# Kernel optimization log

Hardware: AMD Instinct MI355X
Metric: run time of the kernel (lower is better)

## Reference

```python
import jax, jax.numpy as jnp
import numpy as np

S = 1    # support_num
K = 20   # KNN neighbor count for conv layers
B, V = 4, 4096


def _normalize(x, axis):
    n = jnp.linalg.norm(x, axis=axis, keepdims=True)
    return x / jnp.maximum(n, 1e-12)


def _knn(v, k):
    # v: (b, n, 3) -> (b, n, k) indices of k nearest (excluding self)
    sq = jnp.sum(v * v, axis=-1)
    dist = sq[:, :, None] + sq[:, None, :] - 2.0 * jnp.einsum('bic,bjc->bij', v, v)
    return jax.lax.top_k(-dist, k + 1)[1][:, :, 1:]


def _gather(feat, idx):
    # feat (b,n,c), idx (b,n,k) -> (b,n,k,c)
    return feat[jnp.arange(feat.shape[0])[:, None, None], idx]


def _dir_norm(verts, idx):
    nb = _gather(verts, idx)                       # (b,v,k,3)
    return _normalize(nb - verts[:, :, None, :], -1)


def _conv_surface(idx, verts, directions, kernel_num):
    b, v, k = idx.shape
    nd = _dir_norm(verts, idx)
    sd = _normalize(directions, 0)                 # (3, S*kernel_num)
    theta = jax.nn.relu(jnp.einsum('bvkc,cm->bvkm', nd, sd))
    theta = theta.reshape(b, v, k, S, kernel_num)
    return jnp.sum(jnp.max(theta, axis=2), axis=2)  # (b,v,kernel_num)


def _conv_layer(idx, verts, fm, W, bias, directions, out_c):
    b, v, k = idx.shape
    nd = _dir_norm(verts, idx)
    sd = _normalize(directions, 0)                 # (3, S*out_c)
    theta = jax.nn.relu(jnp.einsum('bvkc,cm->bvkm', nd, sd))  # (b,v,k,S*out_c)
    fo = fm @ W + bias                             # (b,v,(S+1)*out_c)
    center = fo[:, :, :out_c]
    support = _gather(fo[:, :, out_c:], idx)       # (b,v,k,S*out_c)
    act = (theta * support).reshape(b, v, k, S, out_c)
    return center + jnp.sum(jnp.max(act, axis=2), axis=2)


def _pool(verts, fm, rate, nn, seed):
    b, v, _ = verts.shape
    idx = _knn(verts, nn)
    pooled = jnp.max(_gather(fm, idx), axis=2)
    sel = jax.random.permutation(jax.random.key(seed), v)[: v // rate]
    return verts[:, sel, :], pooled[:, sel, :]


def _ln(x, g, b):
    m = jnp.mean(x, -1, keepdims=True)
    var = jnp.mean(jnp.square(x - m), -1, keepdims=True)
    return (x - m) / jnp.sqrt(var + 1e-6) * g + b


def _mha(q, kv, Win, bin_, Wout, bout, h):
    E = q.shape[-1]
    hd = E // h
    wq, wk, wv = jnp.split(Win, 3, axis=0)
    bq, bk, bv = jnp.split(bin_, 3)

    def heads(x, w, bb_):
        y = x @ w.T + bb_
        return y.reshape(y.shape[0], y.shape[1], h, hd).transpose(0, 2, 1, 3)

    qh, kh, vh = heads(q, wq, bq), heads(kv, wk, bk), heads(kv, wv, bv)
    a = jax.nn.softmax(jnp.einsum('bhqd,bhkd->bhqk', qh, kh) / jnp.sqrt(jnp.float32(hd)), -1)
    o = jnp.einsum('bhqk,bhkd->bhqd', a, vh).transpose(0, 2, 1, 3).reshape(q.shape)
    return o @ Wout.T + bout


def _conv1x1(x, W, b):
    # x (B,C,N,1) -> (B,O,N,1)
    return jnp.einsum('bcnl,oc->bonl', x, W) + b[None, :, None, None]


def _bn_train(x, g, b):
    # BatchNorm2d in training mode (batch statistics), eps=1e-5
    m = jnp.mean(x, axis=(0, 2, 3), keepdims=True)
    v = jnp.var(x, axis=(0, 2, 3), keepdims=True)
    return (x - m) / jnp.sqrt(v + 1e-5) * g[None, :, None, None] + b[None, :, None, None]


def _forward(vertices, d0, g0, be0, w1, b1, dir1, g1, be1, w2, b2, dir2, g2, be2,
             w3, b3, dir3, g3, be3, token, a1_in_w, a1_in_b, a1_out_w, a1_out_b,
             ffn1_w, ffn1_b, bg, bb, ffn2_w, ffn2_b, a2_in_w, a2_in_b, a2_out_w,
             a2_out_b, w7, b7, dir7, g4, be4, c8_w, c8_b):
    b = vertices.shape[0]
    v0 = vertices[:, 0]                                 # (b, 4096, 3)
    idx0 = _knn(v0, K)
    fm0 = jax.nn.relu(_ln(_conv_surface(idx0, v0, d0, 32), g0, be0))
    fm1 = jax.nn.relu(_ln(_conv_layer(idx0, v0, fm0, w1, b1, dir1, 64), g1, be1))
    v1, fm1 = _pool(v0, fm1, 4, 4, 1)                   # (b,1024,3), (b,1024,64)
    idx1 = _knn(v1, K)
    fm_x = fm1
    fm2 = jax.nn.relu(_ln(_conv_layer(idx1, v1, fm1, w2, b2, dir2, 128), g2, be2))
    fm3 = jax.nn.relu(_ln(_conv_layer(idx1, v1, fm2, w3, b3, dir3, 256), g3, be3))
    _, fm3 = _pool(v1, fm3, 4, 4, 2)                    # (b,256,256)
    tok = jnp.tile(token, (b, 1, 1, 1))[:, :, :, 0].transpose(0, 2, 1)  # (b,1024,64)
    query = _mha(tok, fm_x, a1_in_w, a1_in_b, a1_out_w, a1_out_b, 4) + fm_x
    q2 = query.transpose(0, 2, 1)[:, :, :, None]        # (b,64,1024,1)
    q2 = _conv1x1(jax.nn.relu(_bn_train(_conv1x1(q2, ffn1_w, ffn1_b), bg, bb)), ffn2_w, ffn2_b)
    query = q2[:, :, :, 0].transpose(0, 2, 1)           # (b,1024,256)
    cross = _mha(query, fm3, a2_in_w, a2_in_b, a2_out_w, a2_out_b, 4) + query
    fmf = jax.nn.relu(_ln(_conv_layer(idx1, v1, cross, w7, b7, dir7, 1024), g4, be4))
    fmf = fmf.transpose(0, 2, 1)[:, :, :, None]         # (b,1024,1024,1)
    return _conv1x1(fmf, c8_w, c8_b)                    # (b,256,1024,1)


def setup_inputs():
    ks = iter(jax.random.split(jax.random.key(0), 64))

    def rn(shape, s=0.05):
        return jax.random.normal(next(ks), shape, dtype=jnp.float32) * s

    f32 = jnp.float32
    return dict(
        vertices=jax.random.normal(next(ks), (B, 1, V, 3), dtype=f32),
        d0=rn((3, S * 32)), g0=jnp.ones((32,), f32), be0=jnp.zeros((32,), f32),
        w1=rn((32, (S + 1) * 64)), b1=rn(((S + 1) * 64,)), dir1=rn((3, S * 64)),
        g1=jnp.ones((64,), f32), be1=jnp.zeros((64,), f32),
        w2=rn((64, (S + 1) * 128)), b2=rn(((S + 1) * 128,)), dir2=rn((3, S * 128)),
        g2=jnp.ones((128,), f32), be2=jnp.zeros((128,), f32),
        w3=rn((128, (S + 1) * 256)), b3=rn(((S + 1) * 256,)), dir3=rn((3, S * 256)),
        g3=jnp.ones((256,), f32), be3=jnp.zeros((256,), f32),
        token=rn((1, 64, 1024, 1), 1.0),
        a1_in_w=rn((192, 64)), a1_in_b=rn((192,)), a1_out_w=rn((64, 64)), a1_out_b=rn((64,)),
        ffn1_w=rn((256, 64)), ffn1_b=rn((256,)), bg=jnp.ones((256,), f32), bb=jnp.zeros((256,), f32),
        ffn2_w=rn((256, 256)), ffn2_b=rn((256,)),
        a2_in_w=rn((768, 256)), a2_in_b=rn((768,)), a2_out_w=rn((256, 256)), a2_out_b=rn((256,)),
        w7=rn((256, (S + 1) * 1024)), b7=rn(((S + 1) * 1024,)), dir7=rn((3, S * 1024)),
        g4=jnp.ones((1024,), f32), be4=jnp.zeros((1024,), f32),
        c8_w=rn((256, 1024)), c8_b=rn((256,)),
    )


def reference(vertices, d0, g0, be0, w1, b1, dir1, g1, be1, w2, b2, dir2, g2, be2,
              w3, b3, dir3, g3, be3, token, a1_in_w, a1_in_b, a1_out_w, a1_out_b,
              ffn1_w, ffn1_b, bg, bb, ffn2_w, ffn2_b, a2_in_w, a2_in_b, a2_out_w,
              a2_out_b, w7, b7, dir7, g4, be4, c8_w, c8_b):
    return _forward(vertices, d0, g0, be0, w1, b1, dir1, g1, be1, w2, b2, dir2, g2,
                    be2, w3, b3, dir3, g3, be3, token, a1_in_w, a1_in_b, a1_out_w,
                    a1_out_b, ffn1_w, ffn1_b, bg, bb, ffn2_w, ffn2_b, a2_in_w,
                    a2_in_b, a2_out_w, a2_out_b, w7, b7, dir7, g4, be4, c8_w, c8_b)
```

## Files before the change

kernel.cpp:

```cpp
#include <hip/hip_runtime.h>
#include <stdint.h>
#include <stddef.h>

#define FINF __builtin_inff()

__device__ inline void tf2x32(uint32_t k0, uint32_t k1, uint32_t x0, uint32_t x1,
                              uint32_t* o0, uint32_t* o1) {
  uint32_t ks2 = k0 ^ k1 ^ 0x1BD11BDAu;
  uint32_t v0 = x0 + k0, v1 = x1 + k1;
#define TFR(r) { v0 += v1; v1 = (v1 << (r)) | (v1 >> (32 - (r))); v1 ^= v0; }
  TFR(13) TFR(15) TFR(26) TFR(6)
  v0 += k1;  v1 += ks2 + 1u;
  TFR(17) TFR(29) TFR(16) TFR(24)
  v0 += ks2; v1 += k0 + 2u;
  TFR(13) TFR(15) TFR(26) TFR(6)
  v0 += k0;  v1 += k1 + 3u;
  TFR(17) TFR(29) TFR(16) TFR(24)
  v0 += k1;  v1 += ks2 + 4u;
  TFR(13) TFR(15) TFR(26) TFR(6)
  v0 += ks2; v1 += k0 + 5u;
#undef TFR
  *o0 = v0; *o1 = v1;
}

__device__ inline void perm_subkey(uint32_t seed, int round, uint32_t* s0, uint32_t* s1) {
  uint32_t k0 = 0u, k1 = seed;
  for (int r = 0; r < round; r++) {
    uint32_t a0, a1; tf2x32(k0, k1, 0u, 0u, &a0, &a1);
    k0 = a0; k1 = a1;
  }
  tf2x32(k0, k1, 0u, 1u, s0, s1);
}

__global__ __launch_bounds__(256) void perm_pass_kernel(uint32_t seed, int round, int n,
                                                        const int* __restrict__ vin,
                                                        int* __restrict__ vout, int m) {
  __shared__ unsigned long long lk[4096];
  __shared__ int part[256];
  uint32_t s0, s1; perm_subkey(seed, round, &s0, &s1);
  int t = threadIdx.x;
  for (int j = t; j < n; j += 256) {
    uint32_t y0, y1; tf2x32(s0, s1, 0u, (uint32_t)j, &y0, &y1);
    lk[j] = ((unsigned long long)(y0 ^ y1) << 32) | (unsigned)j;
  }
  __syncthreads();
  int r = blockIdx.x * 64 + (t & 63);
  int q = t >> 6;
  unsigned long long ki = lk[r];
  int cnt = 0;
  int j0 = q * (n >> 2), j1 = j0 + (n >> 2);
  for (int j = j0; j < j1; j++) cnt += (lk[j] < ki) ? 1 : 0;
  part[t] = cnt;
  __syncthreads();
  if (t < 64) {
    int rank = part[t] + part[t + 64] + part[t + 128] + part[t + 192];
    if (rank < m) vout[rank] = vin ? vin[r] : r;
  }
}

__global__ __launch_bounds__(256) void perm_passA_kernel(int* __restrict__ pt1,
                                                         int* __restrict__ sel2) {
  __shared__ unsigned long long lk[4096];
  __shared__ int part[256];
  bool big = (blockIdx.x < 64);
  uint32_t seed = big ? 1u : 2u;
  int n = big ? 4096 : 1024;
  int m = big ? 4096 : 256;
  int* vout = big ? pt1 : sel2;
  int blk = big ? blockIdx.x : (blockIdx.x - 64);
  uint32_t s0, s1; perm_subkey(seed, 0, &s0, &s1);
  int t = threadIdx.x;
  for (int j = t; j < n; j += 256) {
    uint32_t y0, y1; tf2x32(s0, s1, 0u, (uint32_t)j, &y0, &y1);
    lk[j] = ((unsigned long long)(y0 ^ y1) << 32) | (unsigned)j;
  }
  __syncthreads();
  int r = blk * 64 + (t & 63);
  int q = t >> 6;
  unsigned long long ki = lk[r];
  int cnt = 0;
  int j0 = q * (n >> 2), j1 = j0 + (n >> 2);
  for (int j = j0; j < j1; j++) cnt += (lk[j] < ki) ? 1 : 0;
  part[t] = cnt;
  __syncthreads();
  if (t < 64) {
    int rank = part[t] + part[t + 64] + part[t + 128] + part[t + 192];
    if (rank < m) vout[rank] = r;
  }
}

__device__ inline void wave_argmin2(float head_d, int head_i, float* Mo, int* wio) {
  float M = head_d;
#pragma unroll
  for (int off = 1; off < 64; off <<= 1) M = fminf(M, __shfl_xor(M, off));
  int cand = (head_d == M) ? head_i : 0x7fffffff;
#pragma unroll
  for (int off = 1; off < 64; off <<= 1) cand = min(cand, __shfl_xor(cand, off));
  *Mo = M; *wio = cand;
}

template <int CNT, int WAVES>
__global__ __launch_bounds__(64 * WAVES) void knn_lex_kernel(const float* __restrict__ verts,
                                                             int N,
                                                             int* __restrict__ idx20,
                                                             int* __restrict__ idx4) {
  constexpr int SH = (CNT - 1 < 21) ? (CNT - 1) : 21;
  int row = blockIdx.x; int b = row / N, i = row - b * N;
  int t = threadIdx.x; int w = t >> 6; int lane = t & 63;
  const float* vb = verts + (size_t)b * N * 3;
  float xi = vb[i * 3], yi = vb[i * 3 + 1], zi = vb[i * 3 + 2];
  float sqi = (xi * xi + yi * yi) + zi * zi;

  int base = w * (N / WAVES) + lane;
  float qd[CNT]; int qi[CNT];
#pragma unroll
  for (int m = 0; m < CNT; m++) {
    int j = base + m * 64;
    float xj = vb[j * 3], yj = vb[j * 3 + 1], zj = vb[j * 3 + 2];
    float sqj = (xj * xj + yj * yj) + zj * zj;
    float dot = (xi * xj + yi * yj) + zi * zj;
    qd[m] = sqi + sqj - 2.f * dot;
    qi[m] = j;
  }
#pragma unroll
  for (int k = 2; k <= CNT; k <<= 1)
#pragma unroll
    for (int j = k >> 1; j > 0; j >>= 1)
#pragma unroll
      for (int m = 0; m < CNT; m++) {
        int l = m ^ j;
        if (l > m) {
          bool up = ((m & k) == 0);
          bool sw = up ? (qd[m] > qd[l]) : (qd[m] < qd[l]);
          float td = sw ? qd[l] : qd[m]; qd[l] = sw ? qd[m] : qd[l]; qd[m] = td;
          int ti = sw ? qi[l] : qi[m]; qi[l] = sw ? qi[m] : qi[l]; qi[m] = ti;
        }
      }

  __shared__ float wd[WAVES][21];
  __shared__ int wi[WAVES][21];
  for (int r = 0; r < 21; r++) {
    float M; int widx;
    wave_argmin2(qd[0], qi[0], &M, &widx);
    if (lane == 0) { wd[w][r] = M; wi[w][r] = widx; }
    bool win = (qi[0] == widx);
#pragma unroll
    for (int m = 0; m < SH; m++) {
      qd[m] = win ? qd[m + 1] : qd[m];
      qi[m] = win ? qi[m + 1] : qi[m];
    }
    if (SH == CNT - 1) {
      if (win) { qd[CNT - 1] = FINF; qi[CNT - 1] = 0x7fffffff; }
    }
  }
  __syncthreads();
  if (lane < 21) {
    float d0 = wd[w][lane]; int i0 = wi[w][lane];
    int rank = lane;
#pragma unroll
    for (int w2 = 0; w2 < WAVES; w2++) {
      if (w2 == w) continue;
      for (int p = 0; p < 21; p++) {
        float ld = wd[w2][p]; int li = wi[w2][p];
        rank += (ld < d0 || (ld == d0 && li < i0)) ? 1 : 0;
      }
    }
    if (rank >= 1 && rank <= 20) idx20[(size_t)row * 20 + (rank - 1)] = i0;
    if (rank >= 1 && rank <= 4)  idx4[(size_t)row * 4 + (rank - 1)] = i0;
  }
}

__global__ __launch_bounds__(256) void knnv1_w2_kernel(const float* __restrict__ verts,
                                                       int* __restrict__ idx20,
                                                       int* __restrict__ idx4,
                                                       const float* __restrict__ x,
                                                       const float* __restrict__ W,
                                                       const float* __restrict__ bias,
                                                       float* __restrict__ y) {
  if (blockIdx.x < 1024) {
    constexpr int CNT = 16;
    const int N = 1024;
    int lane = threadIdx.x & 63;
    int row = blockIdx.x * 4 + (threadIdx.x >> 6);
    int b = row / N, i = row - b * N;
    const float* vb = verts + (size_t)b * N * 3;
    float xi = vb[i * 3], yi = vb[i * 3 + 1], zi = vb[i * 3 + 2];
    float sqi = (xi * xi + yi * yi) + zi * zi;
    float qd[CNT]; int qi[CNT];
#pragma unroll
    for (int m = 0; m < CNT; m++) {
      int j = lane + m * 64;
      float xj = vb[j * 3], yj = vb[j * 3 + 1], zj = vb[j * 3 + 2];
      float sqj = (xj * xj + yj * yj) + zj * zj;
      float dot = (xi * xj + yi * yj) + zi * zj;
      qd[m] = sqi + sqj - 2.f * dot;
      qi[m] = j;
    }
#pragma unroll
    for (int k = 2; k <= CNT; k <<= 1)
#pragma unroll
      for (int j = k >> 1; j > 0; j >>= 1)
#pragma unroll
        for (int m = 0; m < CNT; m++) {
          int l = m ^ j;
          if (l > m) {
            bool up = ((m & k) == 0);
            bool sw = up ? (qd[m] > qd[l]) : (qd[m] < qd[l]);
            float td = sw ? qd[l] : qd[m]; qd[l] = sw ? qd[m] : qd[l]; qd[m] = td;
            int ti = sw ? qi[l] : qi[m]; qi[l] = sw ? qi[m] : qi[l]; qi[m] = ti;
          }
        }
    for (int r = 0; r < 21; r++) {
      float M; int widx;
      wave_argmin2(qd[0], qi[0], &M, &widx);
      if (lane == 0 && r >= 1) {
        idx20[(size_t)row * 20 + (r - 1)] = widx;
        if (r <= 4) idx4[(size_t)row * 4 + (r - 1)] = widx;
      }
      bool win = (qi[0] == widx);
#pragma unroll
      for (int m = 0; m < CNT - 1; m++) {
        qd[m] = win ? qd[m + 1] : qd[m];
        qi[m] = win ? qi[m + 1] : qi[m];
      }
      if (win) { qd[CNT - 1] = FINF; qi[CNT - 1] = 0x7fffffff; }
    }
  } else {
    const int I = 64, O = 256;
    int rb = (blockIdx.x - 1024) * 8;
    int o = threadIdx.x;
    __shared__ float xs[64][8];
    for (int u = 0; u < 8; u++)
      for (int i2 = threadIdx.x; i2 < I; i2 += 256) xs[i2][u] = x[(size_t)(rb + u) * I + i2];
    __syncthreads();
    float a[8] = {0, 0, 0, 0, 0, 0, 0, 0};
    for (int k2 = 0; k2 < I; k2++) {
      float wv = W[(size_t)k2 * O + o];
      float4 xa = *(const float4*)&xs[k2][0];
      float4 xb = *(const float4*)&xs[k2][4];
      a[0] += xa.x * wv; a[1] += xa.y * wv; a[2] += xa.z * wv; a[3] += xa.w * wv;
      a[4] += xb.x * wv; a[5] += xb.y * wv; a[6] += xb.z * wv; a[7] += xb.w * wv;
    }
    float bv = bias[o];
#pragma unroll
    for (int u = 0; u < 8; u++) y[(size_t)(rb + u) * O + o] = a[u] + bv;
  }
}

__global__ __launch_bounds__(256) void conv_surface_kernel(const float* __restrict__ verts,
                                                           const int* __restrict__ idx20,
                                                           const float* __restrict__ d0,
                                                           const float* __restrict__ g,
                                                           const float* __restrict__ be,
                                                           float* __restrict__ out, int N) {
  int w = threadIdx.x >> 6; int t = threadIdx.x & 63;
  int row = blockIdx.x * 4 + w; int b = row / N, i = row - b * N;
  __shared__ float nd[4][20][3];
  const float* vb = verts + (size_t)b * N * 3;
  if (t < 20) {
    int j = idx20[(size_t)row * 20 + t];
    float dx = vb[j * 3] - vb[i * 3], dy = vb[j * 3 + 1] - vb[i * 3 + 1], dz = vb[j * 3 + 2] - vb[i * 3 + 2];
    float n2 = sqrtf(dx * dx + dy * dy + dz * dz); n2 = fmaxf(n2, 1e-12f);
    nd[w][t][0] = dx / n2; nd[w][t][1] = dy / n2; nd[w][t][2] = dz / n2;
  }
  float x = 0.f;
  if (t < 32) {
    float a = d0[t], bb2 = d0[32 + t], c = d0[64 + t];
    float nrm = fmaxf(sqrtf(a * a + bb2 * bb2 + c * c), 1e-12f);
    a /= nrm; bb2 /= nrm; c /= nrm;
    float mx = -FINF;
    for (int kk = 0; kk < 20; kk++) {
      float th = fmaxf(nd[w][kk][0] * a + nd[w][kk][1] * bb2 + nd[w][kk][2] * c, 0.f);
      mx = fmaxf(mx, th);
    }
    x = mx;
  }
  float s = x;
  for (int off = 32; off; off >>= 1) s += __shfl_xor(s, off);
  float mean = s / 32.f;
  float dev = (t < 32) ? x - mean : 0.f;
  float s2 = dev * dev;
  for (int off = 32; off; off >>= 1) s2 += __shfl_xor(s2, off);
  float var = s2 / 32.f;
  if (t < 32) {
    float y = (x - mean) / sqrtf(var + 1e-6f) * g[t] + be[t];
    out[(size_t)row * 32 + t] = fmaxf(y, 0.f);
  }
}

__global__ void gemm_io_kernel(const float* __restrict__ x, const float* __restrict__ W,
                               const float* __restrict__ bias, float* __restrict__ y,
                               int R, int I, int O) {
  int rb = blockIdx.x * 8;
  int o = blockIdx.y * blockDim.x + threadIdx.x;
  __shared__ float xs[256][8];
  for (int u = 0; u < 8; u++)
    for (int i2 = threadIdx.x; i2 < I; i2 += blockDim.x) xs[i2][u] = x[(size_t)(rb + u) * I + i2];
  __syncthreads();
  float a[8] = {0, 0, 0, 0, 0, 0, 0, 0};
  for (int k2 = 0; k2 < I; k2++) {
    float wv = W[(size_t)k2 * O + o];
    float4 xa = *(const float4*)&xs[k2][0];
    float4 xb = *(const float4*)&xs[k2][4];
    a[0] += xa.x * wv; a[1] += xa.y * wv; a[2] += xa.z * wv; a[3] += xa.w * wv;
    a[4] += xb.x * wv; a[5] += xb.y * wv; a[6] += xb.z * wv; a[7] += xb.w * wv;
  }
  float bv = bias[o];
#pragma unroll
  for (int u = 0; u < 8; u++) y[(size_t)(rb + u) * O + o] = a[u] + bv;
}

__global__ void gemm_io16_kernel(const float* __restrict__ x, const float* __restrict__ W,
                                 const float* __restrict__ bias, float* __restrict__ y,
                                 int R, int I, int O) {
  int rb = blockIdx.x * 16;
  int o = blockIdx.y * blockDim.x + threadIdx.x;
  __shared__ float xs[256][16];
  for (int u = 0; u < 16; u++)
    for (int i2 = threadIdx.x; i2 < I; i2 += blockDim.x) xs[i2][u] = x[(size_t)(rb + u) * I + i2];
  __syncthreads();
  float a[16];
#pragma unroll
  for (int u = 0; u < 16; u++) a[u] = 0.f;
  for (int k2 = 0; k2 < I; k2++) {
    float wv = W[(size_t)k2 * O + o];
    float4 x0 = *(const float4*)&xs[k2][0];
    float4 x1 = *(const float4*)&xs[k2][4];
    float4 x2 = *(const float4*)&xs[k2][8];
    float4 x3 = *(const float4*)&xs[k2][12];
    a[0] += x0.x * wv; a[1] += x0.y * wv; a[2] += x0.z * wv; a[3] += x0.w * wv;
    a[4] += x1.x * wv; a[5] += x1.y * wv; a[6] += x1.z * wv; a[7] += x1.w * wv;
    a[8] += x2.x * wv; a[9] += x2.y * wv; a[10] += x2.z * wv; a[11] += x2.w * wv;
    a[12] += x3.x * wv; a[13] += x3.y * wv; a[14] += x3.z * wv; a[15] += x3.w * wv;
  }
  float bv = bias[o];
#pragma unroll
  for (int u = 0; u < 16; u++) y[(size_t)(rb + u) * O + o] = a[u] + bv;
}

template <int CPT>
__global__ void combine_kernel(const float* __restrict__ verts, const int* __restrict__ idx20,
                               const float* __restrict__ fo, const float* __restrict__ dirs,
                               const float* __restrict__ g, const float* __restrict__ be,
                               float* __restrict__ out, int N, int C) {
  int row = blockIdx.x; int b = row / N, i = row - b * N;
  int t = threadIdx.x, bs = blockDim.x;
  __shared__ float nd[20][3];
  __shared__ int nidx[20];
  __shared__ float red[8];
  const float* vb = verts + (size_t)b * N * 3;
  if (t < 20) {
    int j = idx20[(size_t)row * 20 + t];
    nidx[t] = j;
    float dx = vb[j * 3] - vb[i * 3], dy = vb[j * 3 + 1] - vb[i * 3 + 1], dz = vb[j * 3 + 2] - vb[i * 3 + 2];
    float n2 = fmaxf(sqrtf(dx * dx + dy * dy + dz * dz), 1e-12f);
    nd[t][0] = dx / n2; nd[t][1] = dy / n2; nd[t][2] = dz / n2;
  }
  __syncthreads();
  const float* fob = fo + (size_t)b * N * 2 * C;
  const float* forow = fob + (size_t)i * 2 * C;
  float da[CPT], db[CPT], dc[CPT], mx[CPT];
#pragma unroll
  for (int u = 0; u < CPT; u++) {
    int c = t + u * bs;
    float a = dirs[c], bb = dirs[C + c], cc = dirs[2 * C + c];
    float nrm = fmaxf(sqrtf(a * a + bb * bb + cc * cc), 1e-12f);
    da[u] = a / nrm; db[u] = bb / nrm; dc[u] = cc / nrm;
    mx[u] = -FINF;
  }
  for (int kk = 0; kk < 20; kk++) {
    float n0 = nd[kk][0], n1 = nd[kk][1], n2v = nd[kk][2];
    const float* sup = fob + (size_t)nidx[kk] * 2 * C + C + t;
#pragma unroll
    for (int u = 0; u < CPT; u++) {
      float th = fmaxf(n0 * da[u] + n1 * db[u] + n2v * dc[u], 0.f);
      mx[u] = fmaxf(mx[u], th * sup[u * bs]);
    }
  }
  float xv[CPT];
  float ssum = 0.f;
#pragma unroll
  for (int u = 0; u < CPT; u++) {
    int c = t + u * bs;
    float val = forow[c] + mx[u];
    xv[u] = val; ssum += val;
  }
  int nw = bs >> 6;
  for (int off = 32; off; off >>= 1) ssum += __shfl_down(ssum, off);
  if ((t & 63) == 0) red[t >> 6] = ssum;
  __syncthreads();
  if (t == 0) { float s = red[0]; for (int w = 1; w < nw; w++) s += red[w]; red[0] = s; }
  __syncthreads();
  float mean = red[0] / (float)C;
  __syncthreads();
  float s2 = 0.f;
#pragma unroll
  for (int u = 0; u < CPT; u++) { float d2 = xv[u] - mean; s2 += d2 * d2; }
  for (int off = 32; off; off >>= 1) s2 += __shfl_down(s2, off);
  if ((t & 63) == 0) red[t >> 6] = s2;
  __syncthreads();
  if (t == 0) { float s = red[0]; for (int w = 1; w < nw; w++) s += red[w]; red[0] = s; }
  __syncthreads();
  float inv = 1.0f / sqrtf(red[0] / (float)C + 1e-6f);
#pragma unroll
  for (int u = 0; u < CPT; u++) {
    int c = t + u * bs;
    float yv = (xv[u] - mean) * inv * g[c] + be[c];
    out[(size_t)row * C + c] = fmaxf(yv, 0.f);
  }
}

__global__ void pool_select_kernel(const float* __restrict__ fm, const int* __restrict__ idx4,
                                   const int* __restrict__ sel, const float* __restrict__ vin,
                                   float* __restrict__ vout, float* __restrict__ out,
                                   int N, int M, int C) {
  int row = blockIdx.x; int b = row / M, r = row - b * M;
  int s = sel[r];
  const int* id = idx4 + ((size_t)b * N + s) * 4;
  int i0 = id[0], i1 = id[1], i2 = id[2], i3 = id[3];
  const float* fb = fm + (size_t)b * N * C;
  for (int c = threadIdx.x; c < C; c += blockDim.x) {
    float m = fmaxf(fmaxf(fb[(size_t)i0 * C + c], fb[(size_t)i1 * C + c]),
                    fmaxf(fb[(size_t)i2 * C + c], fb[(size_t)i3 * C + c]));
    out[((size_t)b * M + r) * C + c] = m;
  }
  if (vout != nullptr && threadIdx.x < 3)
    vout[((size_t)b * M + r) * 3 + threadIdx.x] = vin[((size_t)b * N + s) * 3 + threadIdx.x];
}

__global__ void linear_oi_kernel(const float* __restrict__ x, const float* __restrict__ W,
                                 const float* __restrict__ bias, const float* __restrict__ res,
                                 float* __restrict__ y, int R, int I, int O) {
  int rb = blockIdx.x * 8;
  int o = threadIdx.x;
  __shared__ float xs[8][256];
  for (int u = 0; u < 8; u++)
    for (int i2 = threadIdx.x; i2 < I; i2 += O) xs[u][i2] = x[(size_t)(rb + u) * I + i2];
  __syncthreads();
  float a[8] = {0, 0, 0, 0, 0, 0, 0, 0};
  const float* w = W + (size_t)o * I;
  for (int k2 = 0; k2 < I; k2++) {
    float wv = w[k2];
#pragma unroll
    for (int u = 0; u < 8; u++) a[u] += xs[u][k2] * wv;
  }
  float bv = bias[o];
#pragma unroll
  for (int u = 0; u < 8; u++) {
    float val = a[u] + bv;
    if (res) val += res[(size_t)(rb + u) * O + o];
    y[(size_t)(rb + u) * O + o] = val;
  }
}

__global__ void linear_bn_kernel(const float* __restrict__ x, const float* __restrict__ W,
                                 const float* __restrict__ bias,
                                 const float* __restrict__ stats,
                                 const float* __restrict__ g, const float* __restrict__ b2,
                                 float* __restrict__ y, int R, int I, int O) {
  int rb = blockIdx.x * 8;
  int o = threadIdx.x;
  __shared__ float xs[8][256];
  for (int u = 0; u < 8; u++)
    for (int i2 = threadIdx.x; i2 < I; i2 += O) {
      float xr = x[(size_t)(rb + u) * I + i2];
      float yv = (xr - stats[i2]) / sqrtf(stats[I + i2] + 1e-5f) * g[i2] + b2[i2];
      xs[u][i2] = fmaxf(yv, 0.f);
    }
  __syncthreads();
  float a[8] = {0, 0, 0, 0, 0, 0, 0, 0};
  const float* w = W + (size_t)o * I;
  for (int k2 = 0; k2 < I; k2++) {
    float wv = w[k2];
#pragma unroll
    for (int u = 0; u < 8; u++) a[u] += xs[u][k2] * wv;
  }
  float bv = bias[o];
#pragma unroll
  for (int u = 0; u < 8; u++) y[(size_t)(rb + u) * O + o] = a[u] + bv;
}

__global__ __launch_bounds__(64) void qkv1_kernel(const float* __restrict__ token,
                                                  const float* __restrict__ fm1p,
                                                  const float* __restrict__ Win,
                                                  const float* __restrict__ bin,
                                                  float* __restrict__ Q1,
                                                  float* __restrict__ K1,
                                                  float* __restrict__ V1) {
  int ybr = blockIdx.y;
  const float* W = Win + (size_t)ybr * 64 * 64;
  const float* bias = bin + ybr * 64;
  float* out = (ybr == 0) ? Q1 : (ybr == 1) ? K1 : V1;
  int rb = blockIdx.x * 8;
  int o = threadIdx.x;
  __shared__ float xs[8][64];
  if (ybr == 0) {
    for (int u = 0; u < 8; u++) {
      int n = (rb + u) & 1023;
      xs[u][o] = token[(size_t)o * 1024 + n];
    }
  } else {
    for (int u = 0; u < 8; u++) xs[u][o] = fm1p[(size_t)(rb + u) * 64 + o];
  }
  __syncthreads();
  float a[8] = {0, 0, 0, 0, 0, 0, 0, 0};
  const float* w = W + (size_t)o * 64;
  for (int k2 = 0; k2 < 64; k2++) {
    float wv = w[k2];
#pragma unroll
    for (int u = 0; u < 8; u++) a[u] += xs[u][k2] * wv;
  }
  float bv = bias[o];
#pragma unroll
  for (int u = 0; u < 8; u++) out[(size_t)(rb + u) * 64 + o] = a[u] + bv;
}

__global__ __launch_bounds__(256) void kv2_kernel(const float* __restrict__ fm3p,
                                                  const float* __restrict__ Win,
                                                  const float* __restrict__ bin,
                                                  float* __restrict__ K2,
                                                  float* __restrict__ V2) {
  int ybr = blockIdx.y;
  const float* W = Win + (size_t)(1 + ybr) * 256 * 256;
  const float* bias = bin + (1 + ybr) * 256;
  float* out = ybr ? V2 : K2;
  int rb = blockIdx.x * 8;
  int o = threadIdx.x;
  __shared__ float xs[8][256];
  for (int u = 0; u < 8; u++) xs[u][o] = fm3p[(size_t)(rb + u) * 256 + o];
  __syncthreads();
  float a[8] = {0, 0, 0, 0, 0, 0, 0, 0};
  const float* w = W + (size_t)o * 256;
  for (int k2 = 0; k2 < 256; k2++) {
    float wv = w[k2];
#pragma unroll
    for (int u = 0; u < 8; u++) a[u] += xs[u][k2] * wv;
  }
  float bv = bias[o];
#pragma unroll
  for (int u = 0; u < 8; u++) out[(size_t)(rb + u) * 256 + o] = a[u] + bv;
}

template <int HD, int QPT, int KS>
__global__ __launch_bounds__(256) void attn_tiled(
    const float* __restrict__ q, const float* __restrict__ kk,
    const float* __restrict__ vv, float* __restrict__ o,
    int Lq, int Lk, int H, float scale) {
  constexpr int TK = 64;
  constexpr int QG = 256 / (2 * KS);
  constexpr int QPB = QG * QPT;
  constexpr int V4 = HD / 4;
  constexpr int STR = V4 + 1;
  constexpr int HH = HD / 2;
  constexpr int V4H = HH / 4;

  __shared__ float4 Ks[TK * STR];
  __shared__ float4 Vs[TK * STR];

  int t = threadIdx.x;
  int dh = t & 1;
  int ki = (t >> 1) & (KS - 1);
  int qg = t / (2 * KS);
  int nqt = Lq / QPB;
  int qt = blockIdx.x % nqt, bh = blockIdx.x / nqt;
  int h = bh % H, b = bh / H;
  int E = H * HD;
  int q0 = qt * QPB + qg * QPT;

  const float* qbase = q + ((size_t)b * Lq + q0) * E + h * HD + dh * HH;
  const float* kbase = kk + (size_t)b * Lk * E + h * HD;
  const float* vbase = vv + (size_t)b * Lk * E + h * HD;

  float qr[QPT][HH], O[QPT][HH], m[QPT], l[QPT];
#pragma unroll
  for (int r = 0; r < QPT; r++) {
    m[r] = -FINF; l[r] = 0.f;
#pragma unroll
    for (int d = 0; d < HH; d++) { qr[r][d] = qbase[(size_t)r * E + d]; O[r][d] = 0.f; }
  }

  for (int k0 = 0; k0 < Lk; k0 += TK) {
    __syncthreads();
    for (int e = t; e < TK * V4; e += 256) {
      int rr = e / V4, cc = e - rr * V4;
      Ks[rr * STR + cc] = *(const float4*)(kbase + (size_t)(k0 + rr) * E + cc * 4);
      Vs[rr * STR + cc] = *(const float4*)(vbase + (size_t)(k0 + rr) * E + cc * 4);
    }
    __syncthreads();
#pragma unroll 1
    for (int g = 0; g < TK / KS; g += 4) {
      float sc[QPT][4];
#pragma unroll
      for (int jj = 0; jj < 4; jj++) {
        int kl = (g + jj) * KS + ki;
        float sh[QPT];
#pragma unroll
        for (int r = 0; r < QPT; r++) sh[r] = 0.f;
        const float4* kr = &Ks[kl * STR + dh * V4H];
#pragma unroll
        for (int c = 0; c < V4H; c++) {
          float4 kv = kr[c];
#pragma unroll
          for (int r = 0; r < QPT; r++)
            sh[r] += qr[r][4 * c] * kv.x + qr[r][4 * c + 1] * kv.y
                   + qr[r][4 * c + 2] * kv.z + qr[r][4 * c + 3] * kv.w;
        }
#pragma unroll
        for (int r = 0; r < QPT; r++)
          sc[r][jj] = (sh[r] + __shfl_xor(sh[r], 1)) * scale;
      }
#pragma unroll
      for (int r = 0; r < QPT; r++) {
        float tm = fmaxf(fmaxf(sc[r][0], sc[r][1]), fmaxf(sc[r][2], sc[r][3]));
        float nm = fmaxf(m[r], tm);
        float a = __expf(m[r] - nm);
        m[r] = nm;
        float ls = l[r] * a;
#pragma unroll
        for (int d = 0; d < HH; d++) O[r][d] *= a;
#pragma unroll
        for (int jj = 0; jj < 4; jj++) { sc[r][jj] = __expf(sc[r][jj] - nm); ls += sc[r][jj]; }
        l[r] = ls;
      }
#pragma unroll
      for (int jj = 0; jj < 4; jj++) {
        int kl = (g + jj) * KS + ki;
        const float4* vr = &Vs[kl * STR + dh * V4H];
#pragma unroll
        for (int c = 0; c < V4H; c++) {
          float4 v4 = vr[c];
#pragma unroll
          for (int r = 0; r < QPT; r++) {
            O[r][4 * c]     += sc[r][jj] * v4.x;
            O[r][4 * c + 1] += sc[r][jj] * v4.y;
            O[r][4 * c + 2] += sc[r][jj] * v4.z;
            O[r][4 * c + 3] += sc[r][jj] * v4.w;
          }
        }
      }
    }
  }
#pragma unroll
  for (int r = 0; r < QPT; r++) {
    float M = m[r];
#pragma unroll
    for (int mask = 2; mask < 2 * KS; mask <<= 1) M = fmaxf(M, __shfl_xor(M, mask));
    float w = __expf(m[r] - M);
    float ll = l[r] * w;
#pragma unroll
    for (int mask = 2; mask < 2 * KS; mask <<= 1) ll += __shfl_xor(ll, mask);
    float inv = 1.f / ll;
#pragma unroll
    for (int d = 0; d < HH; d++) {
      float x = O[r][d] * w;
#pragma unroll
      for (int mask = 2; mask < 2 * KS; mask <<= 1) x += __shfl_xor(x, mask);
      O[r][d] = x * inv;
    }
  }
  if (ki == 0) {
    float* obase = o + ((size_t)b * Lq + q0) * E + h * HD + dh * HH;
#pragma unroll
    for (int r = 0; r < QPT; r++)
#pragma unroll
      for (int d = 0; d < HH; d++) obase[(size_t)r * E + d] = O[r][d];
  }
}

__global__ void bn_stats_kernel(const float* __restrict__ x, float* __restrict__ stats,
                                int R, int C) {
  int c = blockIdx.x; int t = threadIdx.x;
  __shared__ float red[8];
  float s = 0.f;
  for (int r = t; r < R; r += blockDim.x) s += x[(size_t)r * C + c];
  for (int off = 32; off; off >>= 1) s += __shfl_down(s, off);
  if ((t & 63) == 0) red[t >> 6] = s;
  __syncthreads();
  if (t == 0) { float a = red[0]; for (int w = 1; w < (int)(blockDim.x >> 6); w++) a += red[w]; red[0] = a; }
  __syncthreads();
  float mean = red[0] / (float)R;
  __syncthreads();
  float s2 = 0.f;
  for (int r = t; r < R; r += blockDim.x) { float d = x[(size_t)r * C + c] - mean; s2 += d * d; }
  for (int off = 32; off; off >>= 1) s2 += __shfl_down(s2, off);
  if ((t & 63) == 0) red[t >> 6] = s2;
  __syncthreads();
  if (t == 0) {
    float a = red[0]; for (int w = 1; w < (int)(blockDim.x >> 6); w++) a += red[w];
    stats[c] = mean; stats[C + c] = a / (float)R;
  }
}

__global__ void final_kernel(const float* __restrict__ fmf, const float* __restrict__ W,
                             const float* __restrict__ bias, float* __restrict__ out) {
  int nb = blockIdx.x * 8;
  int o = threadIdx.x;
  __shared__ float xs[1024][8];
  for (int u = 0; u < 8; u++)
    for (int c = threadIdx.x; c < 1024; c += 256) xs[c][u] = fmf[(size_t)(nb + u) * 1024 + c];
  __syncthreads();
  float acc[8] = {0, 0, 0, 0, 0, 0, 0, 0};
  const float* w = W + (size_t)o * 1024;
  for (int c = 0; c < 1024; c++) {
    float wv = w[c];
    float4 xa = *(const float4*)&xs[c][0];
    float4 xb = *(const float4*)&xs[c][4];
    acc[0] += xa.x * wv; acc[1] += xa.y * wv; acc[2] += xa.z * wv; acc[3] += xa.w * wv;
    acc[4] += xb.x * wv; acc[5] += xb.y * wv; acc[6] += xb.z * wv; acc[7] += xb.w * wv;
  }
  float bv = bias[o];
#pragma unroll
  for (int u = 0; u < 8; u++) {
    int r = nb + u; int b = r >> 10; int n = r & 1023;
    out[((size_t)(b * 256 + o) << 10) + n] = acc[u] + bv;
  }
}

extern "C" void kernel_launch(void* const* d_in, const int* in_sizes, int n_in,
                              void* d_out, int out_size, void* d_ws, size_t ws_size,
                              hipStream_t stream) {
  (void)in_sizes; (void)n_in; (void)out_size;
  const float* vertices = (const float*)d_in[0];
  const float* d0       = (const float*)d_in[1];
  const float* g0       = (const float*)d_in[2];
  const float* be0      = (const float*)d_in[3];
  const float* w1       = (const float*)d_in[4];
  const float* b1       = (const float*)d_in[5];
  const float* dir1     = (const float*)d_in[6];
  const float* g1       = (const float*)d_in[7];
  const float* be1      = (const float*)d_in[8];
  const float* w2       = (const float*)d_in[9];
  const float* b2       = (const float*)d_in[10];
  const float* dir2     = (const float*)d_in[11];
  const float* g2       = (const float*)d_in[12];
  const float* be2      = (const float*)d_in[13];
  const float* w3       = (const float*)d_in[14];
  const float* b3       = (const float*)d_in[15];
  const float* dir3     = (const float*)d_in[16];
  const float* g3       = (const float*)d_in[17];
  const float* be3      = (const float*)d_in[18];
  const float* token    = (const float*)d_in[19];
  const float* a1_in_w  = (const float*)d_in[20];
  const float* a1_in_b  = (const float*)d_in[21];
  const float* a1_out_w = (const float*)d_in[22];
  const float* a1_out_b = (const float*)d_in[23];
  const float* ffn1_w   = (const float*)d_in[24];
  const float* ffn1_b   = (const float*)d_in[25];
  const float* bg       = (const float*)d_in[26];
  const float* bbp      = (const float*)d_in[27];
  const float* ffn2_w   = (const float*)d_in[28];
  const float* ffn2_b   = (const float*)d_in[29];
  const float* a2_in_w  = (const float*)d_in[30];
  const float* a2_in_b  = (const float*)d_in[31];
  const float* a2_out_w = (const float*)d_in[32];
  const float* a2_out_b = (const float*)d_in[33];
  const float* w7       = (const float*)d_in[34];
  const float* b7       = (const float*)d_in[35];
  const float* dir7     = (const float*)d_in[36];
  const float* g4       = (const float*)d_in[37];
  const float* be4      = (const float*)d_in[38];
  const float* c8_w     = (const float*)d_in[39];
  const float* c8_b     = (const float*)d_in[40];
  float* out = (float*)d_out;
  float* ws = (float*)d_ws;

  if (ws_size < 78568448u) return;

  float* FO     = ws + 0;
  float* S1     = ws + 8388608;
  float* S2     = ws + 12582912;
  float* S3     = ws + 13631488;
  float* QUERY2 = ws + 14680064;
  float* CROSS  = ws + 15728640;
  float* FM1P   = ws + 16777216;
  float* FM3P   = FM1P + 262144;
  float* TOK    = FM3P + 262144;
  float* Q1     = TOK + 262144;
  float* K1     = Q1 + 262144;
  float* VA1    = K1 + 262144;
  float* ATT1   = VA1 + 262144;
  float* K2     = ATT1 + 262144;
  float* V2     = K2 + 262144;
  float* V1     = V2 + 262144;
  float* BNST   = V1 + 12288;
  int* IDX20_0  = (int*)(BNST + 512);
  int* IDX4_0   = IDX20_0 + 327680;
  int* IDX20_1  = IDX4_0 + 65536;
  int* IDX4_1   = IDX20_1 + 81920;
  int* SEL1     = IDX4_1 + 16384;
  int* SEL2     = SEL1 + 1024;
  int* PT1 = IDX20_0;

  perm_passA_kernel<<<80, 256, 0, stream>>>(PT1, SEL2);
  perm_pass_kernel<<<64, 256, 0, stream>>>(1u, 1, 4096, PT1, SEL1, 1024);

  knn_lex_kernel<32, 2><<<4 * 4096, 128, 0, stream>>>(vertices, 4096, IDX20_0, IDX4_0);
  conv_surface_kernel<<<4096, 256, 0, stream>>>(vertices, IDX20_0, d0, g0, be0, S2, 4096);
  gemm_io_kernel<<<dim3(2048, 1), 128, 0, stream>>>(S2, w1, b1, FO, 16384, 32, 128);
  combine_kernel<1><<<16384, 64, 0, stream>>>(vertices, IDX20_0, FO, dir1, g1, be1, S1, 4096, 64);
  pool_select_kernel<<<4096, 64, 0, stream>>>(S1, IDX4_0, SEL1, vertices, V1, FM1P, 4096, 1024, 64);

  knnv1_w2_kernel<<<1536, 256, 0, stream>>>(V1, IDX20_1, IDX4_1, FM1P, w2, b2, FO);
  combine_kernel<1><<<4096, 128, 0, stream>>>(V1, IDX20_1, FO, dir2, g2, be2, S2, 1024, 128);
  gemm_io_kernel<<<dim3(512, 2), 256, 0, stream>>>(S2, w3, b3, FO, 4096, 128, 512);
  combine_kernel<1><<<4096, 256, 0, stream>>>(V1, IDX20_1, FO, dir3, g3, be3, S3, 1024, 256);
  pool_select_kernel<<<1024, 256, 0, stream>>>(S3, IDX4_1, SEL2, nullptr, nullptr, FM3P, 1024, 256, 256);

  qkv1_kernel<<<dim3(512, 3), 64, 0, stream>>>(token, FM1P, a1_in_w, a1_in_b, Q1, K1, VA1);
  attn_tiled<16, 2, 8><<<512, 256, 0, stream>>>(Q1, K1, VA1, ATT1, 1024, 1024, 4, 0.25f);
  linear_oi_kernel<<<512, 64, 0, stream>>>(ATT1, a1_out_w, a1_out_b, FM1P, S3, 4096, 64, 64);

  linear_oi_kernel<<<512, 256, 0, stream>>>(S3, ffn1_w, ffn1_b, nullptr, S2, 4096, 64, 256);
  bn_stats_kernel<<<256, 256, 0, stream>>>(S2, BNST, 4096, 256);
  linear_bn_kernel<<<512, 256, 0, stream>>>(S2, ffn2_w, ffn2_b, BNST, bg, bbp, QUERY2, 4096, 256, 256);

  linear_oi_kernel<<<512, 256, 0, stream>>>(QUERY2, a2_in_w, a2_in_b, nullptr, S3, 4096, 256, 256);
  kv2_kernel<<<dim3(128, 2), 256, 0, stream>>>(FM3P, a2_in_w, a2_in_b, K2, V2);
  attn_tiled<64, 2, 8><<<512, 256, 0, stream>>>(S3, K2, V2, S1, 1024, 256, 4, 0.125f);
  linear_oi_kernel<<<512, 256, 0, stream>>>(S1, a2_out_w, a2_out_b, QUERY2, CROSS, 4096, 256, 256);

  gemm_io16_kernel<<<dim3(256, 8), 256, 0, stream>>>(CROSS, w7, b7, FO, 4096, 256, 2048);
  combine_kernel<4><<<4096, 256, 0, stream>>>(V1, IDX20_1, FO, dir7, g4, be4, S1, 1024, 1024);
  final_kernel<<<512, 256, 0, stream>>>(S1, c8_w, c8_b, out);
}
```

Measured before the change: 910.7 us.

## Fuse attention-out/FFN linears and register-block output columns in GEMMs

Fuses the first attention output projection with FFN1, and FFN2 (with BN+ReLU applied on load) with the second attention's Q projection, removing two launches and their intermediate global round trips. The layer-3, layer-7 and final GEMMs now compute two or four output columns per thread so each shared-memory activation load feeds more FMAs. BN statistics are computed four channels per block with float4 loads. The multi-column GEMMs use more registers and launch fewer blocks, so occupancy may drop.

```diff
diff --git a/kernel.cpp b/kernel.cpp
--- a/kernel.cpp
+++ b/kernel.cpp
@@ -310,32 +310,69 @@
   for (int u = 0; u < 8; u++) y[(size_t)(rb + u) * O + o] = a[u] + bv;
 }
 
-__global__ void gemm_io16_kernel(const float* __restrict__ x, const float* __restrict__ W,
-                                 const float* __restrict__ bias, float* __restrict__ y,
-                                 int R, int I, int O) {
-  int rb = blockIdx.x * 16;
-  int o = blockIdx.y * blockDim.x + threadIdx.x;
-  __shared__ float xs[256][16];
-  for (int u = 0; u < 16; u++)
-    for (int i2 = threadIdx.x; i2 < I; i2 += blockDim.x) xs[i2][u] = x[(size_t)(rb + u) * I + i2];
-  __syncthreads();
-  float a[16];
-#pragma unroll
-  for (int u = 0; u < 16; u++) a[u] = 0.f;
+__global__ __launch_bounds__(256) void gemm_mc2_kernel(const float* __restrict__ x,
+                                                       const float* __restrict__ W,
+                                                       const float* __restrict__ bias,
+                                                       float* __restrict__ y,
+                                                       int R, int I, int O) {
+  int rb = blockIdx.x * 8;
+  int o = threadIdx.x;
+  __shared__ float xs[256][8];
+  for (int u = 0; u < 8; u++)
+    for (int i2 = threadIdx.x; i2 < I; i2 += 256) xs[i2][u] = x[(size_t)(rb + u) * I + i2];
+  __syncthreads();
+  float a0[8] = {0, 0, 0, 0, 0, 0, 0, 0};
+  float a1[8] = {0, 0, 0, 0, 0, 0, 0, 0};
   for (int k2 = 0; k2 < I; k2++) {
-    float wv = W[(size_t)k2 * O + o];
-    float4 x0 = *(const float4*)&xs[k2][0];
-    float4 x1 = *(const float4*)&xs[k2][4];
-    float4 x2 = *(const float4*)&xs[k2][8];
-    float4 x3 = *(const float4*)&xs[k2][12];
-    a[0] += x0.x * wv; a[1] += x0.y * wv; a[2] += x0.z * wv; a[3] += x0.w * wv;
-    a[4] += x1.x * wv; a[5] += x1.y * wv; a[6] += x1.z * wv; a[7] += x1.w * wv;
-    a[8] += x2.x * wv; a[9] += x2.y * wv; a[10] += x2.z * wv; a[11] += x2.w * wv;
-    a[12] += x3.x * wv; a[13] += x3.y * wv; a[14] += x3.z * wv; a[15] += x3.w * wv;
-  }
-  float bv = bias[o];
-#pragma unroll
-  for (int u = 0; u < 16; u++) y[(size_t)(rb + u) * O + o] = a[u] + bv;
+    float wv0 = W[(size_t)k2 * O + o];
+    float wv1 = W[(size_t)k2 * O + o + 256];
+    float4 xa = *(const float4*)&xs[k2][0];
+    float4 xb = *(const float4*)&xs[k2][4];
+    a0[0] += xa.x * wv0; a0[1] += xa.y * wv0; a0[2] += xa.z * wv0; a0[3] += xa.w * wv0;
+    a0[4] += xb.x * wv0; a0[5] += xb.y * wv0; a0[6] += xb.z * wv0; a0[7] += xb.w * wv0;
+    a1[0] += xa.x * wv1; a1[1] += xa.y * wv1; a1[2] += xa.z * wv1; a1[3] += xa.w * wv1;
+    a1[4] += xb.x * wv1; a1[5] += xb.y * wv1; a1[6] += xb.z * wv1; a1[7] += xb.w * wv1;
+  }
+  float bv0 = bias[o], bv1 = bias[o + 256];
+#pragma unroll
+  for (int u = 0; u < 8; u++) {
+    y[(size_t)(rb + u) * O + o] = a0[u] + bv0;
+    y[(size_t)(rb + u) * O + o + 256] = a1[u] + bv1;
+  }
+}
+
+__global__ __launch_bounds__(256) void gemm_mc4_kernel(const float* __restrict__ x,
+                                                       const float* __restrict__ W,
+                                                       const float* __restrict__ bias,
+                                                       float* __restrict__ y,
+                                                       int R, int I, int O) {
+  int rb = blockIdx.x * 8;
+  int o = blockIdx.y * 1024 + threadIdx.x;
+  __shared__ float xs[256][8];
+  for (int u = 0; u < 8; u++)
+    for (int i2 = threadIdx.x; i2 < I; i2 += 256) xs[i2][u] = x[(size_t)(rb + u) * I + i2];
+  __syncthreads();
+  float a[4][8];
+#pragma unroll
+  for (int m = 0; m < 4; m++)
+#pragma unroll
+    for (int u = 0; u < 8; u++) a[m][u] = 0.f;
+  for (int k2 = 0; k2 < I; k2++) {
+    float4 xa = *(const float4*)&xs[k2][0];
+    float4 xb = *(const float4*)&xs[k2][4];
+#pragma unroll
+    for (int m = 0; m < 4; m++) {
+      float wv = W[(size_t)k2 * O + o + m * 256];
+      a[m][0] += xa.x * wv; a[m][1] += xa.y * wv; a[m][2] += xa.z * wv; a[m][3] += xa.w * wv;
+      a[m][4] += xb.x * wv; a[m][5] += xb.y * wv; a[m][6] += xb.z * wv; a[m][7] += xb.w * wv;
+    }
+  }
+#pragma unroll
+  for (int m = 0; m < 4; m++) {
+    float bv = bias[o + m * 256];
+#pragma unroll
+    for (int u = 0; u < 8; u++) y[(size_t)(rb + u) * O + o + m * 256] = a[m][u] + bv;
+  }
 }
 
 template <int CPT>
@@ -453,31 +490,96 @@
   }
 }
 
-__global__ void linear_bn_kernel(const float* __restrict__ x, const float* __restrict__ W,
-                                 const float* __restrict__ bias,
-                                 const float* __restrict__ stats,
-                                 const float* __restrict__ g, const float* __restrict__ b2,
-                                 float* __restrict__ y, int R, int I, int O) {
+__global__ __launch_bounds__(256) void a1out_ffn1_kernel(const float* __restrict__ att,
+                                                         const float* __restrict__ Wo,
+                                                         const float* __restrict__ bo,
+                                                         const float* __restrict__ res,
+                                                         const float* __restrict__ W1,
+                                                         const float* __restrict__ b1_,
+                                                         float* __restrict__ x1out) {
+  int rb = blockIdx.x * 8;
+  int t = threadIdx.x;
+  __shared__ float xs[8][64];
+  __shared__ float qs[64][8];
+  for (int e = t; e < 512; e += 256) {
+    int u = e >> 6, c = e & 63;
+    xs[u][c] = att[(size_t)(rb + u) * 64 + c];
+  }
+  __syncthreads();
+  for (int e = t; e < 512; e += 256) {
+    int u = e >> 6, o = e & 63;
+    const float* w = Wo + (size_t)o * 64;
+    float acc = 0.f;
+    for (int k = 0; k < 64; k++) acc += xs[u][k] * w[k];
+    float val = acc + bo[o];
+    val += res[(size_t)(rb + u) * 64 + o];
+    qs[o][u] = val;
+  }
+  __syncthreads();
+  float a[8] = {0, 0, 0, 0, 0, 0, 0, 0};
+  const float* w = W1 + (size_t)t * 64;
+  for (int k = 0; k < 64; k++) {
+    float wv = w[k];
+    float4 xa = *(const float4*)&qs[k][0];
+    float4 xb = *(const float4*)&qs[k][4];
+    a[0] += xa.x * wv; a[1] += xa.y * wv; a[2] += xa.z * wv; a[3] += xa.w * wv;
+    a[4] += xb.x * wv; a[5] += xb.y * wv; a[6] += xb.z * wv; a[7] += xb.w * wv;
+  }
+  float bv = b1_[t];
+#pragma unroll
+  for (int u = 0; u < 8; u++) x1out[(size_t)(rb + u) * 256 + t] = a[u] + bv;
+}
+
+__global__ __launch_bounds__(256) void ffn2_q2_kernel(const float* __restrict__ x,
+                                                      const float* __restrict__ W2,
+                                                      const float* __restrict__ b2_,
+                                                      const float* __restrict__ stats,
+                                                      const float* __restrict__ g,
+                                                      const float* __restrict__ bb,
+                                                      const float* __restrict__ Wq,
+                                                      const float* __restrict__ bq,
+                                                      float* __restrict__ query2,
+                                                      float* __restrict__ q2out) {
   int rb = blockIdx.x * 8;
   int o = threadIdx.x;
-  __shared__ float xs[8][256];
-  for (int u = 0; u < 8; u++)
-    for (int i2 = threadIdx.x; i2 < I; i2 += O) {
-      float xr = x[(size_t)(rb + u) * I + i2];
-      float yv = (xr - stats[i2]) / sqrtf(stats[I + i2] + 1e-5f) * g[i2] + b2[i2];
-      xs[u][i2] = fmaxf(yv, 0.f);
-    }
+  __shared__ float xs[256][8];
+  __shared__ float qs[256][8];
+  float mo = stats[o], vo = stats[256 + o], go = g[o], bo = bb[o];
+  for (int u = 0; u < 8; u++) {
+    float xr = x[(size_t)(rb + u) * 256 + o];
+    float yv = (xr - mo) / sqrtf(vo + 1e-5f) * go + bo;
+    xs[o][u] = fmaxf(yv, 0.f);
+  }
   __syncthreads();
   float a[8] = {0, 0, 0, 0, 0, 0, 0, 0};
-  const float* w = W + (size_t)o * I;
-  for (int k2 = 0; k2 < I; k2++) {
-    float wv = w[k2];
-#pragma unroll
-    for (int u = 0; u < 8; u++) a[u] += xs[u][k2] * wv;
-  }
-  float bv = bias[o];
-#pragma unroll
-  for (int u = 0; u < 8; u++) y[(size_t)(rb + u) * O + o] = a[u] + bv;
+  const float* w = W2 + (size_t)o * 256;
+  for (int k = 0; k < 256; k++) {
+    float wv = w[k];
+    float4 xa = *(const float4*)&xs[k][0];
+    float4 xb = *(const float4*)&xs[k][4];
+    a[0] += xa.x * wv; a[1] += xa.y * wv; a[2] += xa.z * wv; a[3] += xa.w * wv;
+    a[4] += xb.x * wv; a[5] += xb.y * wv; a[6] += xb.z * wv; a[7] += xb.w * wv;
+  }
+  float bv = b2_[o];
+#pragma unroll
+  for (int u = 0; u < 8; u++) {
+    float val = a[u] + bv;
+    qs[o][u] = val;
+    query2[(size_t)(rb + u) * 256 + o] = val;
+  }
+  __syncthreads();
+  float c[8] = {0, 0, 0, 0, 0, 0, 0, 0};
+  const float* wq = Wq + (size_t)o * 256;
+  for (int k = 0; k < 256; k++) {
+    float wv = wq[k];
+    float4 xa = *(const float4*)&qs[k][0];
+    float4 xb = *(const float4*)&qs[k][4];
+    c[0] += xa.x * wv; c[1] += xa.y * wv; c[2] += xa.z * wv; c[3] += xa.w * wv;
+    c[4] += xb.x * wv; c[5] += xb.y * wv; c[6] += xb.z * wv; c[7] += xb.w * wv;
+  }
+  float bqv = bq[o];
+#pragma unroll
+  for (int u = 0; u < 8; u++) q2out[(size_t)(rb + u) * 256 + o] = c[u] + bqv;
 }
 
 __global__ __launch_bounds__(64) void qkv1_kernel(const float* __restrict__ token,
@@ -667,52 +769,81 @@
   }
 }
 
-__global__ void bn_stats_kernel(const float* __restrict__ x, float* __restrict__ stats,
-                                int R, int C) {
-  int c = blockIdx.x; int t = threadIdx.x;
-  __shared__ float red[8];
-  float s = 0.f;
-  for (int r = t; r < R; r += blockDim.x) s += x[(size_t)r * C + c];
-  for (int off = 32; off; off >>= 1) s += __shfl_down(s, off);
-  if ((t & 63) == 0) red[t >> 6] = s;
-  __syncthreads();
-  if (t == 0) { float a = red[0]; for (int w = 1; w < (int)(blockDim.x >> 6); w++) a += red[w]; red[0] = a; }
-  __syncthreads();
-  float mean = red[0] / (float)R;
-  __syncthreads();
-  float s2 = 0.f;
-  for (int r = t; r < R; r += blockDim.x) { float d = x[(size_t)r * C + c] - mean; s2 += d * d; }
-  for (int off = 32; off; off >>= 1) s2 += __shfl_down(s2, off);
-  if ((t & 63) == 0) red[t >> 6] = s2;
-  __syncthreads();
-  if (t == 0) {
-    float a = red[0]; for (int w = 1; w < (int)(blockDim.x >> 6); w++) a += red[w];
-    stats[c] = mean; stats[C + c] = a / (float)R;
-  }
-}
-
-__global__ void final_kernel(const float* __restrict__ fmf, const float* __restrict__ W,
-                             const float* __restrict__ bias, float* __restrict__ out) {
+__global__ __launch_bounds__(256) void bn_stats4_kernel(const float* __restrict__ x,
+                                                        float* __restrict__ stats,
+                                                        int R, int C) {
+  int c4 = blockIdx.x * 4;
+  int t = threadIdx.x;
+  __shared__ float red[4][4];
+  __shared__ float mean4[4];
+  float4 s = make_float4(0.f, 0.f, 0.f, 0.f);
+  for (int r = t; r < R; r += 256) {
+    float4 v = *(const float4*)&x[(size_t)r * C + c4];
+    s.x += v.x; s.y += v.y; s.z += v.z; s.w += v.w;
+  }
+  for (int off = 32; off; off >>= 1) {
+    s.x += __shfl_down(s.x, off); s.y += __shfl_down(s.y, off);
+    s.z += __shfl_down(s.z, off); s.w += __shfl_down(s.w, off);
+  }
+  if ((t & 63) == 0) { int w = t >> 6; red[w][0] = s.x; red[w][1] = s.y; red[w][2] = s.z; red[w][3] = s.w; }
+  __syncthreads();
+  if (t < 4) {
+    float a = red[0][t]; a += red[1][t]; a += red[2][t]; a += red[3][t];
+    mean4[t] = a / (float)R;
+  }
+  __syncthreads();
+  float m0 = mean4[0], m1 = mean4[1], m2 = mean4[2], m3 = mean4[3];
+  float4 s2 = make_float4(0.f, 0.f, 0.f, 0.f);
+  for (int r = t; r < R; r += 256) {
+    float4 v = *(const float4*)&x[(size_t)r * C + c4];
+    float d;
+    d = v.x - m0; s2.x += d * d;
+    d = v.y - m1; s2.y += d * d;
+    d = v.z - m2; s2.z += d * d;
+    d = v.w - m3; s2.w += d * d;
+  }
+  for (int off = 32; off; off >>= 1) {
+    s2.x += __shfl_down(s2.x, off); s2.y += __shfl_down(s2.y, off);
+    s2.z += __shfl_down(s2.z, off); s2.w += __shfl_down(s2.w, off);
+  }
+  if ((t & 63) == 0) { int w = t >> 6; red[w][0] = s2.x; red[w][1] = s2.y; red[w][2] = s2.z; red[w][3] = s2.w; }
+  __syncthreads();
+  if (t < 4) {
+    float a = red[0][t]; a += red[1][t]; a += red[2][t]; a += red[3][t];
+    stats[c4 + t] = mean4[t];
+    stats[C + c4 + t] = a / (float)R;
+  }
+}
+
+__global__ __launch_bounds__(128) void final_kernel(const float* __restrict__ fmf,
+                                                    const float* __restrict__ W,
+                                                    const float* __restrict__ bias,
+                                                    float* __restrict__ out) {
   int nb = blockIdx.x * 8;
   int o = threadIdx.x;
   __shared__ float xs[1024][8];
   for (int u = 0; u < 8; u++)
-    for (int c = threadIdx.x; c < 1024; c += 256) xs[c][u] = fmf[(size_t)(nb + u) * 1024 + c];
-  __syncthreads();
-  float acc[8] = {0, 0, 0, 0, 0, 0, 0, 0};
-  const float* w = W + (size_t)o * 1024;
+    for (int c = threadIdx.x; c < 1024; c += 128) xs[c][u] = fmf[(size_t)(nb + u) * 1024 + c];
+  __syncthreads();
+  float a0[8] = {0, 0, 0, 0, 0, 0, 0, 0};
+  float a1[8] = {0, 0, 0, 0, 0, 0, 0, 0};
+  const float* w0 = W + (size_t)o * 1024;
+  const float* w1 = W + (size_t)(o + 128) * 1024;
   for (int c = 0; c < 1024; c++) {
-    float wv = w[c];
+    float wv0 = w0[c], wv1 = w1[c];
     float4 xa = *(const float4*)&xs[c][0];
     float4 xb = *(const float4*)&xs[c][4];
-    acc[0] += xa.x * wv; acc[1] += xa.y * wv; acc[2] += xa.z * wv; acc[3] += xa.w * wv;
-    acc[4] += xb.x * wv; acc[5] += xb.y * wv; acc[6] += xb.z * wv; acc[7] += xb.w * wv;
-  }
-  float bv = bias[o];
+    a0[0] += xa.x * wv0; a0[1] += xa.y * wv0; a0[2] += xa.z * wv0; a0[3] += xa.w * wv0;
+    a0[4] += xb.x * wv0; a0[5] += xb.y * wv0; a0[6] += xb.z * wv0; a0[7] += xb.w * wv0;
+    a1[0] += xa.x * wv1; a1[1] += xa.y * wv1; a1[2] += xa.z * wv1; a1[3] += xa.w * wv1;
+    a1[4] += xb.x * wv1; a1[5] += xb.y * wv1; a1[6] += xb.z * wv1; a1[7] += xb.w * wv1;
+  }
+  float bv0 = bias[o], bv1 = bias[o + 128];
 #pragma unroll
   for (int u = 0; u < 8; u++) {
     int r = nb + u; int b = r >> 10; int n = r & 1023;
-    out[((size_t)(b * 256 + o) << 10) + n] = acc[u] + bv;
+    out[((size_t)(b * 256 + o) << 10) + n] = a0[u] + bv0;
+    out[((size_t)(b * 256 + o + 128) << 10) + n] = a1[u] + bv1;
   }
 }
 
@@ -802,24 +933,23 @@
 
   knnv1_w2_kernel<<<1536, 256, 0, stream>>>(V1, IDX20_1, IDX4_1, FM1P, w2, b2, FO);
   combine_kernel<1><<<4096, 128, 0, stream>>>(V1, IDX20_1, FO, dir2, g2, be2, S2, 1024, 128);
-  gemm_io_kernel<<<dim3(512, 2), 256, 0, stream>>>(S2, w3, b3, FO, 4096, 128, 512);
+  gemm_mc2_kernel<<<512, 256, 0, stream>>>(S2, w3, b3, FO, 4096, 128, 512);
   combine_kernel<1><<<4096, 256, 0, stream>>>(V1, IDX20_1, FO, dir3, g3, be3, S3, 1024, 256);
   pool_select_kernel<<<1024, 256, 0, stream>>>(S3, IDX4_1, SEL2, nullptr, nullptr, FM3P, 1024, 256, 256);
 
   qkv1_kernel<<<dim3(512, 3), 64, 0, stream>>>(token, FM1P, a1_in_w, a1_in_b, Q1, K1, VA1);
   attn_tiled<16, 2, 8><<<512, 256, 0, stream>>>(Q1, K1, VA1, ATT1, 1024, 1024, 4, 0.25f);
-  linear_oi_kernel<<<512, 64, 0, stream>>>(ATT1, a1_out_w, a1_out_b, FM1P, S3, 4096, 64, 64);
-
-  linear_oi_kernel<<<512, 256, 0, stream>>>(S3, ffn1_w, ffn1_b, nullptr, S2, 4096, 64, 256);
-  bn_stats_kernel<<<256, 256, 0, stream>>>(S2, BNST, 4096, 256);
-  linear_bn_kernel<<<512, 256, 0, stream>>>(S2, ffn2_w, ffn2_b, BNST, bg, bbp, QUERY2, 4096, 256, 256);
-
-  linear_oi_kernel<<<512, 256, 0, stream>>>(QUERY2, a2_in_w, a2_in_b, nullptr, S3, 4096, 256, 256);
+  a1out_ffn1_kernel<<<512, 256, 0, stream>>>(ATT1, a1_out_w, a1_out_b, FM1P, ffn1_w, ffn1_b, S2);
+
+  bn_stats4_kernel<<<64, 256, 0, stream>>>(S2, BNST, 4096, 256);
+  ffn2_q2_kernel<<<512, 256, 0, stream>>>(S2, ffn2_w, ffn2_b, BNST, bg, bbp,
+                                          a2_in_w, a2_in_b, QUERY2, S3);
+
   kv2_kernel<<<dim3(128, 2), 256, 0, stream>>>(FM3P, a2_in_w, a2_in_b, K2, V2);
   attn_tiled<64, 2, 8><<<512, 256, 0, stream>>>(S3, K2, V2, S1, 1024, 256, 4, 0.125f);
   linear_oi_kernel<<<512, 256, 0, stream>>>(S1, a2_out_w, a2_out_b, QUERY2, CROSS, 4096, 256, 256);
 
-  gemm_io16_kernel<<<dim3(256, 8), 256, 0, stream>>>(CROSS, w7, b7, FO, 4096, 256, 2048);
+  gemm_mc4_kernel<<<dim3(512, 2), 256, 0, stream>>>(CROSS, w7, b7, FO, 4096, 256, 2048);
   combine_kernel<4><<<4096, 256, 0, stream>>>(V1, IDX20_1, FO, dir7, g4, be4, S1, 1024, 1024);
-  final_kernel<<<512, 256, 0, stream>>>(S1, c8_w, c8_b, out);
-}
+  final_kernel<<<512, 128, 0, stream>>>(S1, c8_w, c8_b, out);
+}
```

After: 886.9 us. -2.6%, faster.
